# Performance work log

Measured on AMD Instinct MI355X. Metric: run time of the kernel, lower is better.

The kernel has to match this reference:

```python
import jax, jax.numpy as jnp
import numpy as np

N_META, M_SUB = 64, 1024          # n meta-nodes, m nodes per sub-graph
D_IN, D_HID, D_OUT = 128, 128, 64
NUM_LAYERS_EXTRA, K = 2, 3        # total DSGraphGLayers = NUM_LAYERS_EXTRA + 1
N_EDGES = 1048576                 # ~avg degree 16 over 65536 nodes


def setup_inputs() -> dict:
    key = jax.random.key(0)
    ks = jax.random.split(key, 8)
    N = N_META * M_SUB
    x = jax.random.normal(ks[0], (N_META, M_SUB, D_IN), jnp.float32)
    sub_adj = jax.random.randint(ks[1], (2, N_EDGES), 0, N, dtype=jnp.int32)
    # dense binary meta-graph adjacency (n, n)
    adj = (jax.random.uniform(ks[2], (N_META, N_META)) < 0.1).astype(jnp.float32)
    L = NUM_LAYERS_EXTRA + 1
    scale = 1.0 / np.sqrt(D_HID).astype(np.float32)
    gcn_W = jax.random.normal(ks[3], (L, K + 1, D_HID, D_HID), jnp.float32) * scale
    gcn_b = jnp.zeros((L, K + 1, D_HID), jnp.float32)
    lin_W1 = jax.random.normal(ks[4], (D_HID, D_HID), jnp.float32) * scale
    lin_b1 = jnp.zeros((D_HID,), jnp.float32)
    lin_W2 = jax.random.normal(ks[5], (D_HID, D_OUT), jnp.float32) * scale
    lin_b2 = jnp.zeros((D_OUT,), jnp.float32)
    return dict(x=x, sub_adj=sub_adj, adj=adj, gcn_W=gcn_W, gcn_b=gcn_b,
                lin_W1=lin_W1, lin_b1=lin_b1, lin_W2=lin_W2, lin_b2=lin_b2)


def _gcn_conv(x, src, dst, dinv, W, b, N):
    norm = dinv[src] * dinv[dst]                      # [E+N]
    msg = (x @ W)[src] * norm[:, None]                # [E+N, d_out]
    return jax.ops.segment_sum(msg, dst, num_segments=N) + b


def reference(x, sub_adj, adj, gcn_W, gcn_b, lin_W1, lin_b1, lin_W2, lin_b2):
    n, m, d = x.shape
    N = n * m
    loops = jnp.arange(N, dtype=sub_adj.dtype)
    src = jnp.concatenate([sub_adj[0], loops])
    dst = jnp.concatenate([sub_adj[1], loops])
    deg = jax.ops.segment_sum(jnp.ones(src.shape, x.dtype), dst, num_segments=N)
    dinv = jnp.where(deg > 0, jax.lax.rsqrt(deg), jnp.zeros_like(deg))
    # precompute_adj: cached_adj = [adj, adj^2, ..., adj^K]; powers >= 2 detached in source
    cached = [adj]
    A = adj
    for _ in range(K - 1):
        A = jax.lax.stop_gradient(A @ adj)
        cached.append(A)
    for li in range(gcn_W.shape[0]):
        xf = x.reshape(N, -1)
        out = _gcn_conv(xf, src, dst, dinv, gcn_W[li, 0], gcn_b[li, 0], N)
        for i, Ai in enumerate(cached):
            # meta-graph mixing: x_i[n,m,d] = sum_j A_i[n,j] * x[j,m,d]
            xi = jnp.einsum('nj,jmd->nmd', Ai, x).reshape(N, -1)
            out = out + _gcn_conv(xi, src, dst, dinv, gcn_W[li, i + 1], gcn_b[li, i + 1], N)
        x = jax.nn.relu(out.reshape(n, m, -1))
    h = x.reshape(N, -1)
    h = jax.nn.relu(h @ lin_W1 + lin_b1)
    h = h @ lin_W2 + lin_b2
    return h.reshape(n, m, -1)
```

## Files before the change

kernel.cpp:

```cpp
#include <hip/hip_runtime.h>

#define NMETA 64
#define MSUB 1024
#define NNODES 65536
#define D 128
#define DOUT 64
#define NEDGES 1048576
#define COLS 131072
#define BCAP 5120

typedef __attribute__((ext_vector_type(8))) short bf8_t;
typedef __attribute__((ext_vector_type(4))) float f4_t;
typedef __attribute__((ext_vector_type(2))) float f2_t;
typedef __attribute__((ext_vector_type(2))) unsigned ui2_t;

__device__ inline unsigned short bfr(float x) {
    unsigned u = __builtin_bit_cast(unsigned, x);
    u += 0x7fffu + ((u >> 16) & 1u);
    return (unsigned short)(u >> 16);
}
__device__ inline float b2f(unsigned short h) {
    return __builtin_bit_cast(float, (unsigned)h << 16);
}
__device__ inline f2_t up2(unsigned u) {
    f2_t r;
    r[0] = __builtin_bit_cast(float, u << 16);
    r[1] = __builtin_bit_cast(float, u & 0xffff0000u);
    return r;
}

__global__ __launch_bounds__(256) void k_bhist(const int* __restrict__ dst,
                                               int* __restrict__ whist) {
    __shared__ int c[256];
    int t = threadIdx.x, w = blockIdx.x;
    c[t] = 0;
    __syncthreads();
    const int* dp = dst + w * 4096;
    for (int k = 0; k < 16; ++k) atomicAdd(&c[dp[k * 256 + t] >> 8], 1);
    __syncthreads();
    whist[t * 256 + w] = c[t];
}

__global__ __launch_bounds__(256) void k_bscan(int* __restrict__ whist,
                                               int* __restrict__ bbase) {
    __shared__ int sh[256];
    int t = threadIdx.x;
    int run = 0;
    for (int w = 0; w < 256; ++w) {
        int v = whist[t * 256 + w];
        whist[t * 256 + w] = run;
        run += v;
    }
    sh[t] = run;
    __syncthreads();
    for (int d = 1; d < 256; d <<= 1) {
        int x = (t >= d) ? sh[t - d] : 0;
        __syncthreads();
        sh[t] += x;
        __syncthreads();
    }
    bbase[t] = sh[t] - run;
    if (t == 255) bbase[256] = NEDGES;
}

__global__ __launch_bounds__(256) void k_bscatter(const int* __restrict__ src,
                                                  const int* __restrict__ dst,
                                                  const int* __restrict__ bbase,
                                                  const int* __restrict__ whist,
                                                  unsigned* __restrict__ tmp) {
    __shared__ int cur[256];
    __shared__ int base[256];
    int t = threadIdx.x, w = blockIdx.x;
    cur[t] = 0;
    base[t] = bbase[t] + whist[t * 256 + w];
    __syncthreads();
    const int* dp = dst + w * 4096;
    const int* sp = src + w * 4096;
    for (int k = 0; k < 16; ++k) {
        int d = dp[k * 256 + t], s = sp[k * 256 + t];
        int b = d >> 8;
        int lr = atomicAdd(&cur[b], 1);
        tmp[base[b] + lr] = ((unsigned)(d & 255) << 16) | (unsigned)s;
    }
}

__global__ __launch_bounds__(256) void k_bcsr(const unsigned* __restrict__ tmp,
                                              const int* __restrict__ bbase,
                                              int* __restrict__ offs,
                                              float* __restrict__ dinv,
                                              unsigned short* __restrict__ csr16) {
    __shared__ unsigned pairs[BCAP];
    __shared__ unsigned short image[BCAP];
    __shared__ int cnt[256], cur[256], sh[256];
    int t = threadIdx.x, b = blockIdx.x;
    int base = bbase[b], n = bbase[b + 1] - base;
    for (int i = t; i < n; i += 256) pairs[i] = tmp[base + i];
    cnt[t] = 0;
    __syncthreads();
    for (int i = t; i < n; i += 256) atomicAdd(&cnt[pairs[i] >> 16], 1);
    __syncthreads();
    int c = cnt[t];
    sh[t] = c;
    __syncthreads();
    for (int d = 1; d < 256; d <<= 1) {
        int x = (t >= d) ? sh[t - d] : 0;
        __syncthreads();
        sh[t] += x;
        __syncthreads();
    }
    int excl = sh[t] - c;
    cur[t] = excl;
    offs[b * 256 + t] = base + excl;
    dinv[b * 256 + t] = rsqrtf((float)(c + 1));
    if (b == 255 && t == 255) offs[65536] = NEDGES;
    __syncthreads();
    for (int i = t; i < n; i += 256) {
        unsigned p = pairs[i];
        int pos = atomicAdd(&cur[p >> 16], 1);
        image[pos] = (unsigned short)(p & 0xffffu);
    }
    __syncthreads();
    for (int i = t; i < n; i += 256) csr16[base + i] = image[i];
}

__global__ __launch_bounds__(256) void k_setup(const float* __restrict__ A,
                                               unsigned short* __restrict__ Ab,
                                               const float* __restrict__ gcnW,
                                               const float* __restrict__ W1,
                                               const float* __restrict__ W2,
                                               const float* __restrict__ gcnB,
                                               unsigned short* __restrict__ Wt,
                                               float* __restrict__ bsum) {
    int blk = blockIdx.x, t = threadIdx.x;
    if (blk == 0) {
        __shared__ float As[4096];
        __shared__ float Bs[4096];
        for (int q = 0; q < 16; ++q) As[t + 256 * q] = A[t + 256 * q];
        __syncthreads();
        for (int q = 0; q < 16; ++q) {
            int idx = t + 256 * q;
            int n = idx >> 6, j = idx & 63;
            Ab[idx] = bfr(As[idx]);
            float acc = 0.f;
            for (int k = 0; k < 64; ++k) acc += As[n * 64 + k] * As[k * 64 + j];
            Bs[idx] = acc;
            Ab[4096 + idx] = bfr(acc);
        }
        __syncthreads();
        for (int q = 0; q < 16; ++q) {
            int idx = t + 256 * q;
            int n = idx >> 6, j = idx & 63;
            float acc = 0.f;
            for (int k = 0; k < 64; ++k) acc += Bs[n * 64 + k] * As[k * 64 + j];
            Ab[8192 + idx] = bfr(acc);
        }
        if (t < 128) {
            for (int li = 0; li < 3; ++li) {
                const float* bp = gcnB + li * 512 + t;
                bsum[li * 128 + t] = bp[0] + bp[128] + bp[256] + bp[384];
            }
        }
    } else {
        int b2 = blk - 1;
        int m = b2 >> 6;
        int idx = (b2 & 63) * 256 + t;
        const float* src;
        int N = 128;
        if (m < 12)       src = gcnW + m * 16384;
        else if (m == 12) src = W1;
        else { src = W2; N = 64; if (idx >= 8192) return; }
        int n = idx >> 7, k = idx & 127;
        Wt[m * 16384 + idx] = bfr(src[k * N + n]);
    }
}

template <bool INF32>
__global__ __launch_bounds__(256) void k_layer(const unsigned short* __restrict__ X,
                                               const float* __restrict__ Xf,
                                               const unsigned short* __restrict__ Ab,
                                               const unsigned short* __restrict__ Wt4,
                                               const float* __restrict__ dinv,
                                               unsigned short* __restrict__ Y) {
    __shared__ unsigned short LB[8192];
    __shared__ float dsh[64];
    int t = threadIdx.x;
    int m = blockIdx.x;
    int wave = t >> 6, lane = t & 63;
    int l16 = lane & 15, kg = lane >> 4;
    int c0 = wave * 32;

    if (t < 64) dsh[t] = dinv[(long)t * MSUB + m];

#pragma unroll
    for (int it = 0; it < 4; ++it) {
        int slot = it * 256 + t;
        int row = slot >> 4, ch = slot & 15;
        if (INF32) {
            const float* xp = Xf + ((long)row * MSUB + m) * D + ch * 8;
            float4 va = *(const float4*)xp;
            float4 vb = *(const float4*)(xp + 4);
            uint4 pk;
            pk.x = ((unsigned)bfr(va.y) << 16) | bfr(va.x);
            pk.y = ((unsigned)bfr(va.w) << 16) | bfr(va.z);
            pk.z = ((unsigned)bfr(vb.y) << 16) | bfr(vb.x);
            pk.w = ((unsigned)bfr(vb.w) << 16) | bfr(vb.z);
            *(uint4*)&LB[row * 128 + ch * 8] = pk;
        } else {
            *(uint4*)&LB[row * 128 + ch * 8] =
                *(const uint4*)(X + ((long)row * MSUB + m) * D + ch * 8);
        }
    }
    __syncthreads();

    bf8_t xa[4][4];
#pragma unroll
    for (int mt = 0; mt < 4; ++mt)
#pragma unroll
        for (int kb = 0; kb < 4; ++kb)
            xa[mt][kb] = *(const bf8_t*)&LB[(mt * 16 + l16) * 128 + kb * 32 + kg * 8];
    __syncthreads();

    f4_t zero4 = {0.f, 0.f, 0.f, 0.f};

    f4_t acc2[4][2];
#pragma unroll
    for (int mt = 0; mt < 4; ++mt)
#pragma unroll
        for (int nt = 0; nt < 2; ++nt) acc2[mt][nt] = zero4;
#pragma unroll
    for (int kb = 0; kb < 4; ++kb)
#pragma unroll
        for (int nt = 0; nt < 2; ++nt) {
            bf8_t b = *(const bf8_t*)(Wt4 + (long)(c0 + nt * 16 + l16) * 128 +
                                      kb * 32 + kg * 8);
#pragma unroll
            for (int mt = 0; mt < 4; ++mt)
                acc2[mt][nt] = __builtin_amdgcn_mfma_f32_16x16x32_bf16(
                    xa[mt][kb], b, acc2[mt][nt], 0, 0, 0);
        }

    char* slab = (char*)&LB[wave * 2048];
    const unsigned swz = (unsigned)((l16 & 7) << 4);
#pragma unroll
    for (int z = 1; z < 4; ++z) {
        f4_t acc[4][2];
#pragma unroll
        for (int mt = 0; mt < 4; ++mt)
#pragma unroll
            for (int nt = 0; nt < 2; ++nt) acc[mt][nt] = zero4;
        const unsigned short* wp = Wt4 + z * 16384;
#pragma unroll
        for (int kb = 0; kb < 4; ++kb)
#pragma unroll
            for (int nt = 0; nt < 2; ++nt) {
                bf8_t b = *(const bf8_t*)(wp + (long)(c0 + nt * 16 + l16) * 128 +
                                          kb * 32 + kg * 8);
#pragma unroll
                for (int mt = 0; mt < 4; ++mt)
                    acc[mt][nt] = __builtin_amdgcn_mfma_f32_16x16x32_bf16(
                        xa[mt][kb], b, acc[mt][nt], 0, 0, 0);
            }
#pragma unroll
        for (int mt = 0; mt < 4; ++mt)
#pragma unroll
            for (int nt = 0; nt < 2; ++nt) {
                unsigned lo = (unsigned)bfr(acc[mt][nt][0]) |
                              ((unsigned)bfr(acc[mt][nt][1]) << 16);
                unsigned hi = (unsigned)bfr(acc[mt][nt][2]) |
                              ((unsigned)bfr(acc[mt][nt][3]) << 16);
                ui2_t pk = {lo, hi};
                unsigned boff =
                    (unsigned)(((nt * 16 + l16) * 64 + mt * 16 + kg * 4) * 2) ^ swz;
                *(ui2_t*)(slab + boff) = pk;
            }
        int i = z - 1;
#pragma unroll
        for (int kb = 0; kb < 2; ++kb) {
            bf8_t af[4];
#pragma unroll
            for (int mt = 0; mt < 4; ++mt)
                af[mt] = *(const bf8_t*)(Ab + i * 4096 + (mt * 16 + l16) * 64 +
                                         kb * 32 + kg * 8);
#pragma unroll
            for (int nt = 0; nt < 2; ++nt) {
                unsigned boff =
                    (unsigned)(((nt * 16 + l16) * 64 + kb * 32 + kg * 8) * 2) ^ swz;
                bf8_t b = *(const bf8_t*)(slab + boff);
#pragma unroll
                for (int mt = 0; mt < 4; ++mt)
                    acc2[mt][nt] = __builtin_amdgcn_mfma_f32_16x16x32_bf16(
                        af[mt], b, acc2[mt][nt], 0, 0, 0);
            }
        }
    }

#pragma unroll
    for (int mt = 0; mt < 4; ++mt)
#pragma unroll
        for (int nt = 0; nt < 2; ++nt)
#pragma unroll
            for (int r = 0; r < 4; ++r) {
                int row = mt * 16 + kg * 4 + r;
                int col = c0 + nt * 16 + l16;
                float v = acc2[mt][nt][r] * dsh[row];
                Y[((long)row * MSUB + m) * D + col] = bfr(v);
            }
}

__global__ __launch_bounds__(256) void k_prop(const unsigned short* __restrict__ Y,
                                              const int* __restrict__ offs,
                                              const unsigned short* __restrict__ csr,
                                              const float* __restrict__ dinv,
                                              const float* __restrict__ bsum,
                                              unsigned short* __restrict__ Xout) {
    int wid = threadIdx.x >> 6;
    int lane = threadIdx.x & 63;
    int q = lane >> 4;
    int l = lane & 15;
    int v = blockIdx.x * 4 + wid;
    const uint4* Y4 = (const uint4*)Y;
    int e0 = offs[v], e1 = offs[v + 1];
    f2_t acc2[4];
#pragma unroll
    for (int k = 0; k < 4; ++k) acc2[k] = (f2_t){0.f, 0.f};

    int e = e0 + q;
    for (; e + 4 < e1; e += 8) {
        int u0 = __builtin_nontemporal_load(csr + e);
        int u1 = __builtin_nontemporal_load(csr + e + 4);
        uint4 y0 = Y4[(long)u0 * 16 + l];
        uint4 y1 = Y4[(long)u1 * 16 + l];
        acc2[0] += up2(y0.x) + up2(y1.x);
        acc2[1] += up2(y0.y) + up2(y1.y);
        acc2[2] += up2(y0.z) + up2(y1.z);
        acc2[3] += up2(y0.w) + up2(y1.w);
    }
    if (e < e1) {
        int u = __builtin_nontemporal_load(csr + e);
        uint4 y = Y4[(long)u * 16 + l];
        acc2[0] += up2(y.x);
        acc2[1] += up2(y.y);
        acc2[2] += up2(y.z);
        acc2[3] += up2(y.w);
    }
    float acc[8];
#pragma unroll
    for (int k = 0; k < 4; ++k) { acc[2 * k] = acc2[k][0]; acc[2 * k + 1] = acc2[k][1]; }
#pragma unroll
    for (int k = 0; k < 8; ++k) {
        acc[k] += __shfl_xor(acc[k], 32, 64);
        acc[k] += __shfl_xor(acc[k], 16, 64);
    }
    if (q == 0) {
        float dv = dinv[v];
        uint4 s = Y4[(long)v * 16 + l];
        f2_t s2[4] = {up2(s.x), up2(s.y), up2(s.z), up2(s.w)};
        float4 blo = *(const float4*)(bsum + l * 8);
        float4 bhi = *(const float4*)(bsum + l * 8 + 4);
        float bs[8] = {blo.x, blo.y, blo.z, blo.w, bhi.x, bhi.y, bhi.z, bhi.w};
        unsigned r[8];
#pragma unroll
        for (int k = 0; k < 8; ++k) {
            float sf = s2[k / 2][k % 2];
            r[k] = bfr(fmaxf(dv * (acc[k] + sf) + bs[k], 0.f));
        }
        uint4 pk;
        pk.x = (r[1] << 16) | r[0];
        pk.y = (r[3] << 16) | r[2];
        pk.z = (r[5] << 16) | r[4];
        pk.w = (r[7] << 16) | r[6];
        ((uint4*)Xout)[(long)v * 16 + l] = pk;
    }
}

#define HST 136
__global__ __launch_bounds__(256) void k_mlp(const unsigned short* __restrict__ X,
                                             const unsigned short* __restrict__ Wt,
                                             const float* __restrict__ b1,
                                             const float* __restrict__ b2,
                                             float* __restrict__ out) {
    __shared__ unsigned short H[128 * HST];
    int wave = threadIdx.x >> 6, lane = threadIdx.x & 63;
    int l16 = lane & 15, kg = lane >> 4;
    long row0 = (long)blockIdx.x * 128 + wave * 32;
    int hb = wave * 32 * HST;

    bf8_t a[2][4];
    const unsigned short* xp = X + row0 * 128 + kg * 8;
#pragma unroll
    for (int kb = 0; kb < 4; ++kb) {
        a[0][kb] = *(const bf8_t*)(xp + (long)l16 * 128 + kb * 32);
        a[1][kb] = *(const bf8_t*)(xp + (long)(l16 + 16) * 128 + kb * 32);
    }
    f4_t zero4 = {0.f, 0.f, 0.f, 0.f};
    f4_t acc[2][8];
#pragma unroll
    for (int mt = 0; mt < 2; ++mt)
#pragma unroll
        for (int nt = 0; nt < 8; ++nt) acc[mt][nt] = zero4;

    const unsigned short* wp = Wt + 12 * 16384 + (long)l16 * 128 + kg * 8;
#pragma unroll
    for (int kb = 0; kb < 4; ++kb)
#pragma unroll
        for (int nt = 0; nt < 8; ++nt) {
            bf8_t b = *(const bf8_t*)(wp + nt * 16 * 128 + kb * 32);
            acc[0][nt] = __builtin_amdgcn_mfma_f32_16x16x32_bf16(a[0][kb], b, acc[0][nt], 0, 0, 0);
            acc[1][nt] = __builtin_amdgcn_mfma_f32_16x16x32_bf16(a[1][kb], b, acc[1][nt], 0, 0, 0);
        }

#pragma unroll
    for (int nt = 0; nt < 8; ++nt) {
        float bv = b1[nt * 16 + l16];
#pragma unroll
        for (int mt = 0; mt < 2; ++mt)
#pragma unroll
            for (int r = 0; r < 4; ++r) {
                int row = mt * 16 + kg * 4 + r;
                H[hb + row * HST + nt * 16 + l16] = bfr(fmaxf(acc[mt][nt][r] + bv, 0.f));
            }
    }

    bf8_t h2[2][4];
#pragma unroll
    for (int kb = 0; kb < 4; ++kb) {
        h2[0][kb] = *(const bf8_t*)&H[hb + l16 * HST + kb * 32 + kg * 8];
        h2[1][kb] = *(const bf8_t*)&H[hb + (l16 + 16) * HST + kb * 32 + kg * 8];
    }
    f4_t acc2[2][4];
#pragma unroll
    for (int mt = 0; mt < 2; ++mt)
#pragma unroll
        for (int nt = 0; nt < 4; ++nt) acc2[mt][nt] = zero4;
    const unsigned short* w2 = Wt + 13 * 16384 + (long)l16 * 128 + kg * 8;
#pragma unroll
    for (int kb = 0; kb < 4; ++kb)
#pragma unroll
        for (int nt = 0; nt < 4; ++nt) {
            bf8_t b = *(const bf8_t*)(w2 + nt * 16 * 128 + kb * 32);
            acc2[0][nt] = __builtin_amdgcn_mfma_f32_16x16x32_bf16(h2[0][kb], b, acc2[0][nt], 0, 0, 0);
            acc2[1][nt] = __builtin_amdgcn_mfma_f32_16x16x32_bf16(h2[1][kb], b, acc2[1][nt], 0, 0, 0);
        }
#pragma unroll
    for (int mt = 0; mt < 2; ++mt)
#pragma unroll
        for (int nt = 0; nt < 4; ++nt)
#pragma unroll
            for (int r = 0; r < 4; ++r) {
                long row = row0 + mt * 16 + kg * 4 + r;
                int col = nt * 16 + l16;
                out[row * DOUT + col] = acc2[mt][nt][r] + b2[col];
            }
}

extern "C" void kernel_launch(void* const* d_in, const int* in_sizes, int n_in,
                              void* d_out, int out_size, void* d_ws, size_t ws_size,
                              hipStream_t stream) {
    const float* x      = (const float*)d_in[0];
    const int*   subadj = (const int*)d_in[1];
    const float* adj    = (const float*)d_in[2];
    const float* gcn_W  = (const float*)d_in[3];
    const float* gcn_b  = (const float*)d_in[4];
    const float* lin_W1 = (const float*)d_in[5];
    const float* lin_b1 = (const float*)d_in[6];
    const float* lin_W2 = (const float*)d_in[7];
    const float* lin_b2 = (const float*)d_in[8];
    float* out = (float*)d_out;

    const int* e_src = subadj;
    const int* e_dst = subadj + NEDGES;

    char* w = (char*)d_ws;
    int*      whist = (int*)w;      w += (size_t)65536 * 4;
    int*      bbase = (int*)w;      w += (size_t)260 * 4;
    int*      offs  = (int*)w;      w += (size_t)65540 * 4;
    float*    dinv  = (float*)w;    w += (size_t)65536 * 4;
    unsigned* tmp   = (unsigned*)w; w += (size_t)NEDGES * 4;
    unsigned short* csr16 = (unsigned short*)w; w += (size_t)NEDGES * 2;
    unsigned short* Ab  = (unsigned short*)w; w += (size_t)3 * 4096 * 2;
    unsigned short* Xbf = (unsigned short*)w; w += (size_t)NNODES * D * 2;
    unsigned short* Ybf = (unsigned short*)w; w += (size_t)NNODES * D * 2;
    unsigned short* Wt  = (unsigned short*)w; w += (size_t)14 * 16384 * 2;
    float*    bsum  = (float*)w;    w += (size_t)3 * 128 * 4;

    k_bhist<<<256, 256, 0, stream>>>(e_dst, whist);
    k_bscan<<<1, 256, 0, stream>>>(whist, bbase);
    k_bscatter<<<256, 256, 0, stream>>>(e_src, e_dst, bbase, whist, tmp);
    k_bcsr<<<256, 256, 0, stream>>>(tmp, bbase, offs, dinv, csr16);
    k_setup<<<897, 256, 0, stream>>>(adj, Ab, gcn_W, lin_W1, lin_W2, gcn_b,
                                     Wt, bsum);

    for (int li = 0; li < 3; ++li) {
        if (li == 0)
            k_layer<true><<<MSUB, 256, 0, stream>>>(nullptr, x, Ab, Wt, dinv, Ybf);
        else
            k_layer<false><<<MSUB, 256, 0, stream>>>(Xbf, nullptr, Ab,
                                                     Wt + (size_t)li * 4 * 16384, dinv, Ybf);
        k_prop<<<NNODES / 4, 256, 0, stream>>>(Ybf, offs, csr16, dinv,
                                               bsum + (size_t)li * 128, Xbf);
    }
    k_mlp<<<NNODES / 128, 256, 0, stream>>>(Xbf, Wt, lin_b1, lin_b2, out);
}
```

Baseline: 430.0 us.

## Split Y into two 64-column planes and propagate each half separately

The layer kernel now writes its bf16 output as two planes of 64 columns each, and the propagation kernel launches twice as many blocks, each handling one plane. Each gather touches 128 bytes instead of 256, and 8 edges are processed in parallel per wave instead of 4. The smaller planes (8 MB each) are meant to fit better in cache during the random neighbor gather. In exchange the CSR index list and offsets are read twice, and the reduction needs an extra shuffle stage.

Measured after the change: 480.3 us. 11.7% more time.

```diff
diff --git a/kernel.cpp b/kernel.cpp
--- a/kernel.cpp
+++ b/kernel.cpp
@@ -8,6 +8,7 @@
 #define NEDGES 1048576
 #define COLS 131072
 #define BCAP 5120
+#define YPL ((size_t)NNODES * 64)
 
 typedef __attribute__((ext_vector_type(8))) short bf8_t;
 typedef __attribute__((ext_vector_type(4))) float f4_t;
@@ -294,6 +295,8 @@
         }
     }
 
+    unsigned short* Yp = Y + (size_t)(wave >> 1) * YPL;
+    int cc0 = (wave & 1) * 32;
 #pragma unroll
     for (int mt = 0; mt < 4; ++mt)
 #pragma unroll
@@ -301,9 +304,9 @@
 #pragma unroll
             for (int r = 0; r < 4; ++r) {
                 int row = mt * 16 + kg * 4 + r;
-                int col = c0 + nt * 16 + l16;
+                int cc = cc0 + nt * 16 + l16;
                 float v = acc2[mt][nt][r] * dsh[row];
-                Y[((long)row * MSUB + m) * D + col] = bfr(v);
+                Yp[((long)row * MSUB + m) * 64 + cc] = bfr(v);
             }
 }
 
@@ -315,21 +318,22 @@
                                               unsigned short* __restrict__ Xout) {
     int wid = threadIdx.x >> 6;
     int lane = threadIdx.x & 63;
-    int q = lane >> 4;
-    int l = lane & 15;
-    int v = blockIdx.x * 4 + wid;
-    const uint4* Y4 = (const uint4*)Y;
+    int slot = lane >> 3;
+    int l = lane & 7;
+    int pl = blockIdx.x & 1;
+    int v = (blockIdx.x >> 1) * 4 + wid;
+    const uint4* Yp = (const uint4*)(Y + (size_t)pl * YPL);
     int e0 = offs[v], e1 = offs[v + 1];
     f2_t acc2[4];
 #pragma unroll
     for (int k = 0; k < 4; ++k) acc2[k] = (f2_t){0.f, 0.f};
 
-    int e = e0 + q;
-    for (; e + 4 < e1; e += 8) {
+    int e = e0 + slot;
+    for (; e + 8 < e1; e += 16) {
         int u0 = __builtin_nontemporal_load(csr + e);
-        int u1 = __builtin_nontemporal_load(csr + e + 4);
-        uint4 y0 = Y4[(long)u0 * 16 + l];
-        uint4 y1 = Y4[(long)u1 * 16 + l];
+        int u1 = __builtin_nontemporal_load(csr + e + 8);
+        uint4 y0 = Yp[(long)u0 * 8 + l];
+        uint4 y1 = Yp[(long)u1 * 8 + l];
         acc2[0] += up2(y0.x) + up2(y1.x);
         acc2[1] += up2(y0.y) + up2(y1.y);
         acc2[2] += up2(y0.z) + up2(y1.z);
@@ -337,7 +341,7 @@
     }
     if (e < e1) {
         int u = __builtin_nontemporal_load(csr + e);
-        uint4 y = Y4[(long)u * 16 + l];
+        uint4 y = Yp[(long)u * 8 + l];
         acc2[0] += up2(y.x);
         acc2[1] += up2(y.y);
         acc2[2] += up2(y.z);
@@ -348,15 +352,16 @@
     for (int k = 0; k < 4; ++k) { acc[2 * k] = acc2[k][0]; acc[2 * k + 1] = acc2[k][1]; }
 #pragma unroll
     for (int k = 0; k < 8; ++k) {
+        acc[k] += __shfl_xor(acc[k], 8, 64);
+        acc[k] += __shfl_xor(acc[k], 16, 64);
         acc[k] += __shfl_xor(acc[k], 32, 64);
-        acc[k] += __shfl_xor(acc[k], 16, 64);
-    }
-    if (q == 0) {
+    }
+    if (slot == 0) {
         float dv = dinv[v];
-        uint4 s = Y4[(long)v * 16 + l];
+        uint4 s = Yp[(long)v * 8 + l];
         f2_t s2[4] = {up2(s.x), up2(s.y), up2(s.z), up2(s.w)};
-        float4 blo = *(const float4*)(bsum + l * 8);
-        float4 bhi = *(const float4*)(bsum + l * 8 + 4);
+        float4 blo = *(const float4*)(bsum + pl * 64 + l * 8);
+        float4 bhi = *(const float4*)(bsum + pl * 64 + l * 8 + 4);
         float bs[8] = {blo.x, blo.y, blo.z, blo.w, bhi.x, bhi.y, bhi.z, bhi.w};
         unsigned r[8];
 #pragma unroll
@@ -369,7 +374,7 @@
         pk.y = (r[3] << 16) | r[2];
         pk.z = (r[5] << 16) | r[4];
         pk.w = (r[7] << 16) | r[6];
-        ((uint4*)Xout)[(long)v * 16 + l] = pk;
+        ((uint4*)Xout)[(long)v * 16 + pl * 8 + l] = pk;
     }
 }
 
@@ -496,8 +501,8 @@
         else
             k_layer<false><<<MSUB, 256, 0, stream>>>(Xbf, nullptr, Ab,
                                                      Wt + (size_t)li * 4 * 16384, dinv, Ybf);
-        k_prop<<<NNODES / 4, 256, 0, stream>>>(Ybf, offs, csr16, dinv,
-                                               bsum + (size_t)li * 128, Xbf);
+        k_prop<<<(NNODES / 4) * 2, 256, 0, stream>>>(Ybf, offs, csr16, dinv,
+                                                     bsum + (size_t)li * 128, Xbf);
     }
     k_mlp<<<NNODES / 128, 256, 0, stream>>>(Xbf, Wt, lin_b1, lin_b2, out);
 }
```
